# Optimization experiments

Hardware: AMD Instinct MI355X
Metric: run time of the kernel (lower is better)

Reference implementation:

```python
import jax, jax.numpy as jnp
import numpy as np

N_TGT = 100000
DEG = 16
N_EDGE = N_TGT * DEG
N_NBR = 200000
F_IN = 128
F_OUT = 128


def setup_inputs() -> dict:
    key = jax.random.key(0)
    k1, k2, k3, k4, k5, k6 = jax.random.split(key, 6)
    csr_row_ptr = (jnp.arange(N_TGT + 1, dtype=jnp.int64 if jax.config.x64_enabled else jnp.int32) * DEG).astype(jnp.int32)
    csr_col_ind = jax.random.randint(k1, (N_EDGE,), 0, N_NBR, dtype=jnp.int32)
    sample_count = jax.random.randint(k2, (N_NBR,), 0, DEG, dtype=jnp.int32)
    x_neighboor = jax.random.normal(k3, (N_NBR, F_IN), dtype=jnp.float32)
    x_target = jax.random.normal(k4, (N_TGT, F_IN), dtype=jnp.float32)
    # Linear(in=2*F_IN, out=F_OUT): xavier_uniform weight (gain for relu = sqrt(2)),
    # default torch Linear bias init U(-1/sqrt(fan_in), 1/sqrt(fan_in)).
    fan_in = 2 * F_IN
    gain = float(np.sqrt(2.0))
    bound_w = gain * float(np.sqrt(6.0 / (fan_in + F_OUT)))
    lin_weight = jax.random.uniform(k5, (F_OUT, fan_in), dtype=jnp.float32, minval=-bound_w, maxval=bound_w)
    bound_b = 1.0 / float(np.sqrt(fan_in))
    lin_bias = jax.random.uniform(k6, (F_OUT,), dtype=jnp.float32, minval=-bound_b, maxval=bound_b)
    bias = jnp.zeros((F_OUT,), dtype=jnp.float32)  # extra self.bias Parameter (zeros)
    return {
        "csr_row_ptr": csr_row_ptr,
        "csr_col_ind": csr_col_ind,
        "sample_count": sample_count,
        "x_neighboor": x_neighboor,
        "x_target": x_target,
        "lin_weight": lin_weight,
        "lin_bias": lin_bias,
        "bias": bias,
    }


def _mean_aggregate(csr_row_ptr, csr_col_ind, x_neighboor):
    n_tgt = csr_row_ptr.shape[0] - 1
    n_edge = csr_col_ind.shape[0]
    # row id for each edge: which CSR segment it falls into
    edge_ids = jnp.arange(n_edge, dtype=csr_row_ptr.dtype)
    row_ids = jnp.searchsorted(csr_row_ptr, edge_ids, side="right") - 1
    gathered = x_neighboor[csr_col_ind]                      # [E, F]
    summed = jax.ops.segment_sum(gathered, row_ids, num_segments=n_tgt)  # [N, F]
    counts = (csr_row_ptr[1:] - csr_row_ptr[:-1]).astype(x_neighboor.dtype)
    counts = jnp.maximum(counts, 1.0)
    return summed / counts[:, None]


def reference(csr_row_ptr, csr_col_ind, sample_count, x_neighboor, x_target, lin_weight, lin_bias, bias):
    agg = _mean_aggregate(csr_row_ptr, csr_col_ind, x_neighboor)        # [N, F_IN]
    cat = jnp.concatenate([x_target, agg], axis=1)                       # [N, 2*F_IN]
    y = cat @ lin_weight.T + lin_bias
    y = y + bias  # module adds its own self.bias on top of Linear's bias
    return y
```

## Files before the change

kernel.cpp:

```cpp
#include <hip/hip_runtime.h>

#define TM 64
#define F_INC 128
#define K_DIM 256
#define F_OUTC 128
#define CAT_LD 264

using fv2    = __attribute__((ext_vector_type(2))) float;
using fv4    = __attribute__((ext_vector_type(4))) float;
using f32x4  = __attribute__((ext_vector_type(4))) float;
using bf16x8 = __attribute__((ext_vector_type(8))) short;
using u16x8  = __attribute__((ext_vector_type(8))) unsigned short;

static __device__ __forceinline__ unsigned short f2bf(float f) {
    union { float f; unsigned u; } v; v.f = f;
    unsigned u = v.u;
    u += 0x7FFFu + ((u >> 16) & 1u);
    return (unsigned short)(u >> 16);
}

__global__ __launch_bounds__(256) void f32_to_bf16_kernel(
    const float* __restrict__ src, unsigned short* __restrict__ dst, int n8)
{
    const int i = blockIdx.x * 256 + threadIdx.x;
    if (i < n8) {
        const fv4 a = *(const fv4*)(src + (size_t)i * 8);
        const fv4 b = *(const fv4*)(src + (size_t)i * 8 + 4);
        u16x8 o;
        o[0] = f2bf(a[0]); o[1] = f2bf(a[1]); o[2] = f2bf(a[2]); o[3] = f2bf(a[3]);
        o[4] = f2bf(b[0]); o[5] = f2bf(b[1]); o[6] = f2bf(b[2]); o[7] = f2bf(b[3]);
        *(u16x8*)(dst + (size_t)i * 8) = o;
    }
}

__global__ __launch_bounds__(256) void f32_to_fp8_kernel(
    const float* __restrict__ src, unsigned int* __restrict__ dst, int n8)
{
    const int i = blockIdx.x * 256 + threadIdx.x;
    if (i < n8) {
        const fv4 a = *(const fv4*)(src + (size_t)i * 8);
        const fv4 b = *(const fv4*)(src + (size_t)i * 8 + 4);
        unsigned int w0 = (unsigned)__builtin_amdgcn_cvt_pk_fp8_f32(a[0], a[1], 0, false);
        w0 = (unsigned)__builtin_amdgcn_cvt_pk_fp8_f32(a[2], a[3], (int)w0, true);
        unsigned int w1 = (unsigned)__builtin_amdgcn_cvt_pk_fp8_f32(b[0], b[1], 0, false);
        w1 = (unsigned)__builtin_amdgcn_cvt_pk_fp8_f32(b[2], b[3], (int)w1, true);
        uint2 o; o.x = w0; o.y = w1;
        *(uint2*)(dst + (size_t)i * 2) = o;
    }
}

template <int USE_WS>
__global__ __launch_bounds__(256) void sage_fused_kernel(
    const int* __restrict__ row_ptr,
    const int* __restrict__ col_ind,
    const float* __restrict__ x_nbr,
    const unsigned int* __restrict__ nbr_f8,
    const float* __restrict__ x_tgt,
    const float* __restrict__ w,
    const unsigned short* __restrict__ w_bf,
    const float* __restrict__ lin_b,
    const float* __restrict__ bias,
    float* __restrict__ out,
    int n_tgt)
{
    __shared__ int s_ptr[TM + 1];
    __shared__ int s_idx[TM * 16];
    __shared__ unsigned short s_cat[TM][CAT_LD];

    const int tid = threadIdx.x;
    const int g0  = blockIdx.x * TM;

    if (tid < TM + 1) {
        int gp = g0 + tid;
        if (gp > n_tgt) gp = n_tgt;
        s_ptr[tid] = row_ptr[gp];
    }
    __syncthreads();

    for (int e = tid; e < TM * 16; e += 256) {
        const int m = e >> 4, j = e & 15;
        const int start = s_ptr[m];
        const int deg = s_ptr[m + 1] - start;
        s_idx[e] = (j < deg) ? col_ind[start + j] : 0;
    }
    __syncthreads();

    if (USE_WS) {
        const int team = tid >> 3;
        const int lt   = tid & 7;
        for (int mi = 0; mi < 2; ++mi) {
            const int m  = team + mi * 32;
            const int gm = g0 + m;
            {
                u16x8 t0 = {0,0,0,0,0,0,0,0}, t1 = {0,0,0,0,0,0,0,0};
                if (gm < n_tgt) {
                    const float* tp = x_tgt + (size_t)gm * F_INC + lt * 16;
                    const fv4 a = *(const fv4*)(tp);
                    const fv4 b = *(const fv4*)(tp + 4);
                    const fv4 c = *(const fv4*)(tp + 8);
                    const fv4 d = *(const fv4*)(tp + 12);
                    t0[0]=f2bf(a[0]); t0[1]=f2bf(a[1]); t0[2]=f2bf(a[2]); t0[3]=f2bf(a[3]);
                    t0[4]=f2bf(b[0]); t0[5]=f2bf(b[1]); t0[6]=f2bf(b[2]); t0[7]=f2bf(b[3]);
                    t1[0]=f2bf(c[0]); t1[1]=f2bf(c[1]); t1[2]=f2bf(c[2]); t1[3]=f2bf(c[3]);
                    t1[4]=f2bf(d[0]); t1[5]=f2bf(d[1]); t1[6]=f2bf(d[2]); t1[7]=f2bf(d[3]);
                }
                *(u16x8*)&s_cat[m][lt * 16]     = t0;
                *(u16x8*)&s_cat[m][lt * 16 + 8] = t1;
            }
            const int deg = s_ptr[m + 1] - s_ptr[m];
            float acc[16];
#pragma unroll
            for (int i = 0; i < 16; ++i) acc[i] = 0.f;
            const int* idx = &s_idx[m * 16];
            if (deg == 16) {
#pragma unroll
                for (int j = 0; j < 16; ++j) {
                    const uint4 v = *(const uint4*)(nbr_f8 + (size_t)idx[j] * 32 + lt * 4);
                    fv2 p;
                    p = __builtin_amdgcn_cvt_pk_f32_fp8(v.x, false); acc[0]+=p[0];  acc[1]+=p[1];
                    p = __builtin_amdgcn_cvt_pk_f32_fp8(v.x, true ); acc[2]+=p[0];  acc[3]+=p[1];
                    p = __builtin_amdgcn_cvt_pk_f32_fp8(v.y, false); acc[4]+=p[0];  acc[5]+=p[1];
                    p = __builtin_amdgcn_cvt_pk_f32_fp8(v.y, true ); acc[6]+=p[0];  acc[7]+=p[1];
                    p = __builtin_amdgcn_cvt_pk_f32_fp8(v.z, false); acc[8]+=p[0];  acc[9]+=p[1];
                    p = __builtin_amdgcn_cvt_pk_f32_fp8(v.z, true ); acc[10]+=p[0]; acc[11]+=p[1];
                    p = __builtin_amdgcn_cvt_pk_f32_fp8(v.w, false); acc[12]+=p[0]; acc[13]+=p[1];
                    p = __builtin_amdgcn_cvt_pk_f32_fp8(v.w, true ); acc[14]+=p[0]; acc[15]+=p[1];
                }
            } else {
                for (int j = 0; j < deg; ++j) {
                    const uint4 v = *(const uint4*)(nbr_f8 + (size_t)idx[j] * 32 + lt * 4);
                    fv2 p;
                    p = __builtin_amdgcn_cvt_pk_f32_fp8(v.x, false); acc[0]+=p[0];  acc[1]+=p[1];
                    p = __builtin_amdgcn_cvt_pk_f32_fp8(v.x, true ); acc[2]+=p[0];  acc[3]+=p[1];
                    p = __builtin_amdgcn_cvt_pk_f32_fp8(v.y, false); acc[4]+=p[0];  acc[5]+=p[1];
                    p = __builtin_amdgcn_cvt_pk_f32_fp8(v.y, true ); acc[6]+=p[0];  acc[7]+=p[1];
                    p = __builtin_amdgcn_cvt_pk_f32_fp8(v.z, false); acc[8]+=p[0];  acc[9]+=p[1];
                    p = __builtin_amdgcn_cvt_pk_f32_fp8(v.z, true ); acc[10]+=p[0]; acc[11]+=p[1];
                    p = __builtin_amdgcn_cvt_pk_f32_fp8(v.w, false); acc[12]+=p[0]; acc[13]+=p[1];
                    p = __builtin_amdgcn_cvt_pk_f32_fp8(v.w, true ); acc[14]+=p[0]; acc[15]+=p[1];
                }
            }
            const float sc = 1.0f / (float)(deg > 0 ? deg : 1);
            u16x8 p0, p1;
#pragma unroll
            for (int i = 0; i < 8; ++i) { p0[i] = f2bf(acc[i] * sc); p1[i] = f2bf(acc[8 + i] * sc); }
            *(u16x8*)&s_cat[m][128 + lt * 16]     = p0;
            *(u16x8*)&s_cat[m][128 + lt * 16 + 8] = p1;
        }
    } else {
        const int lane32 = tid & 31;
        const int grp = tid >> 5;
        for (int m = grp; m < TM; m += 8) {
            const int gm = g0 + m;
            fv4 t = {0.f, 0.f, 0.f, 0.f};
            if (gm < n_tgt)
                t = *(const fv4*)(x_tgt + (size_t)gm * F_INC + lane32 * 4);
            {
                ushort4 p;
                p.x = f2bf(t[0]); p.y = f2bf(t[1]); p.z = f2bf(t[2]); p.w = f2bf(t[3]);
                *(ushort4*)&s_cat[m][lane32 * 4] = p;
            }
            const int deg = s_ptr[m + 1] - s_ptr[m];
            fv4 acc = {0.f, 0.f, 0.f, 0.f};
            const int* idx = &s_idx[m * 16];
            if (deg == 16) {
#pragma unroll
                for (int j = 0; j < 16; ++j)
                    acc += *(const fv4*)(x_nbr + (size_t)idx[j] * F_INC + lane32 * 4);
            } else {
                for (int j = 0; j < deg; ++j)
                    acc += *(const fv4*)(x_nbr + (size_t)idx[j] * F_INC + lane32 * 4);
            }
            const float sc = 1.0f / (float)(deg > 0 ? deg : 1);
            acc *= sc;
            {
                ushort4 p;
                p.x = f2bf(acc[0]); p.y = f2bf(acc[1]); p.z = f2bf(acc[2]); p.w = f2bf(acc[3]);
                *(ushort4*)&s_cat[m][128 + lane32 * 4] = p;
            }
        }
    }
    __syncthreads();

    const int lane = tid & 63;
    const int wave = tid >> 6;
    const int col  = lane & 15;
    const int kq   = lane >> 4;
    const int r0   = kq * 4;

    bf16x8 bfr[2][8];
#pragma unroll
    for (int h = 0; h < 2; ++h) {
        const int o = h * 64 + wave * 16 + col;
#pragma unroll
        for (int kt = 0; kt < 8; ++kt) {
            if (USE_WS) {
                bfr[h][kt] = *(const bf16x8*)(w_bf + (size_t)o * K_DIM + kt * 32 + kq * 8);
            } else {
                const float* p = w + (size_t)o * K_DIM + kt * 32 + kq * 8;
                fv4 lo = *(const fv4*)p;
                fv4 hi = *(const fv4*)(p + 4);
                bf16x8 b;
                b[0] = (short)f2bf(lo[0]); b[1] = (short)f2bf(lo[1]);
                b[2] = (short)f2bf(lo[2]); b[3] = (short)f2bf(lo[3]);
                b[4] = (short)f2bf(hi[0]); b[5] = (short)f2bf(hi[1]);
                b[6] = (short)f2bf(hi[2]); b[7] = (short)f2bf(hi[3]);
                bfr[h][kt] = b;
            }
        }
    }

    const int o0 = wave * 16 + col;
    const int o1 = 64 + o0;
    const float bs0 = lin_b[o0] + bias[o0];
    const float bs1 = lin_b[o1] + bias[o1];

#pragma unroll 1
    for (int mt = 0; mt < 4; ++mt) {
        const int mrow = mt * 16 + col;
        bf16x8 afr[8];
#pragma unroll
        for (int kt = 0; kt < 8; ++kt)
            afr[kt] = *(const bf16x8*)&s_cat[mrow][kt * 32 + kq * 8];

        f32x4 acc0 = {0.f, 0.f, 0.f, 0.f};
        f32x4 acc1 = {0.f, 0.f, 0.f, 0.f};
#pragma unroll
        for (int kt = 0; kt < 8; ++kt) {
            acc0 = __builtin_amdgcn_mfma_f32_16x16x32_bf16(afr[kt], bfr[0][kt], acc0, 0, 0, 0);
            acc1 = __builtin_amdgcn_mfma_f32_16x16x32_bf16(afr[kt], bfr[1][kt], acc1, 0, 0, 0);
        }

#pragma unroll
        for (int i = 0; i < 4; ++i) {
            const int gm = g0 + mt * 16 + r0 + i;
            if (gm < n_tgt) {
                out[(size_t)gm * F_OUTC + o0] = acc0[i] + bs0;
                out[(size_t)gm * F_OUTC + o1] = acc1[i] + bs1;
            }
        }
    }
}

extern "C" void kernel_launch(void* const* d_in, const int* in_sizes, int n_in,
                              void* d_out, int out_size, void* d_ws, size_t ws_size,
                              hipStream_t stream) {
    const int*   row_ptr = (const int*)d_in[0];
    const int*   col_ind = (const int*)d_in[1];
    const float* x_nbr   = (const float*)d_in[3];
    const float* x_tgt   = (const float*)d_in[4];
    const float* w       = (const float*)d_in[5];
    const float* lb      = (const float*)d_in[6];
    const float* bs      = (const float*)d_in[7];
    float* out = (float*)d_out;

    const int n_tgt  = in_sizes[0] - 1;
    const int n_nbrf = in_sizes[3];
    const int n_wf   = in_sizes[5];
    const int grid   = (n_tgt + TM - 1) / TM;

    const size_t nbr_bytes = (size_t)n_nbrf;
    const size_t need = nbr_bytes + (size_t)n_wf * 2;

    if (ws_size >= need) {
        unsigned int*   nbr_f8 = (unsigned int*)d_ws;
        unsigned short* w_bf   = (unsigned short*)((char*)d_ws + nbr_bytes);
        const int n8n = n_nbrf / 8;
        const int n8w = n_wf / 8;
        hipLaunchKernelGGL(f32_to_fp8_kernel, dim3((n8n + 255) / 256), dim3(256), 0, stream,
                           x_nbr, nbr_f8, n8n);
        hipLaunchKernelGGL(f32_to_bf16_kernel, dim3((n8w + 255) / 256), dim3(256), 0, stream,
                           w, w_bf, n8w);
        hipLaunchKernelGGL(sage_fused_kernel<1>, dim3(grid), dim3(256), 0, stream,
                           row_ptr, col_ind, x_nbr, nbr_f8, x_tgt, w, w_bf, lb, bs, out, n_tgt);
    } else {
        hipLaunchKernelGGL(sage_fused_kernel<0>, dim3(grid), dim3(256), 0, stream,
                           row_ptr, col_ind, x_nbr, (const unsigned int*)nullptr,
                           x_tgt, w, (const unsigned short*)nullptr, lb, bs, out, n_tgt);
    }
}
```

Baseline: 84.33 us.

## Halve target tile, merge conversion kernels, cut register use in MFMA stage

Merges the fp8 neighbour conversion and the bf16 weight conversion into a single launch, which removes one kernel launch. Halves the per-block target tile to 32 rows, so each thread gathers one row instead of two and the grid doubles. The MFMA stage now keeps only one half of the weight fragments live at a time and loads A fragments inside the loop, which lowers register pressure to raise occupancy. The cost is that each block loads the weights and biases for half as many rows, so weight reloads per output row double.

```diff
diff --git a/kernel.cpp b/kernel.cpp
--- a/kernel.cpp
+++ b/kernel.cpp
@@ -1,6 +1,6 @@
 #include <hip/hip_runtime.h>
 
-#define TM 64
+#define TM 32
 #define F_INC 128
 #define K_DIM 256
 #define F_OUTC 128
@@ -19,33 +19,30 @@
     return (unsigned short)(u >> 16);
 }
 
-__global__ __launch_bounds__(256) void f32_to_bf16_kernel(
-    const float* __restrict__ src, unsigned short* __restrict__ dst, int n8)
+__global__ __launch_bounds__(256) void convert_kernel(
+    const float* __restrict__ xn, unsigned int* __restrict__ nf8, int n8n,
+    const float* __restrict__ w, unsigned short* __restrict__ wbf, int n8w)
 {
     const int i = blockIdx.x * 256 + threadIdx.x;
-    if (i < n8) {
-        const fv4 a = *(const fv4*)(src + (size_t)i * 8);
-        const fv4 b = *(const fv4*)(src + (size_t)i * 8 + 4);
-        u16x8 o;
-        o[0] = f2bf(a[0]); o[1] = f2bf(a[1]); o[2] = f2bf(a[2]); o[3] = f2bf(a[3]);
-        o[4] = f2bf(b[0]); o[5] = f2bf(b[1]); o[6] = f2bf(b[2]); o[7] = f2bf(b[3]);
-        *(u16x8*)(dst + (size_t)i * 8) = o;
-    }
-}
-
-__global__ __launch_bounds__(256) void f32_to_fp8_kernel(
-    const float* __restrict__ src, unsigned int* __restrict__ dst, int n8)
-{
-    const int i = blockIdx.x * 256 + threadIdx.x;
-    if (i < n8) {
-        const fv4 a = *(const fv4*)(src + (size_t)i * 8);
-        const fv4 b = *(const fv4*)(src + (size_t)i * 8 + 4);
+    if (i < n8n) {
+        const fv4 a = *(const fv4*)(xn + (size_t)i * 8);
+        const fv4 b = *(const fv4*)(xn + (size_t)i * 8 + 4);
         unsigned int w0 = (unsigned)__builtin_amdgcn_cvt_pk_fp8_f32(a[0], a[1], 0, false);
         w0 = (unsigned)__builtin_amdgcn_cvt_pk_fp8_f32(a[2], a[3], (int)w0, true);
         unsigned int w1 = (unsigned)__builtin_amdgcn_cvt_pk_fp8_f32(b[0], b[1], 0, false);
         w1 = (unsigned)__builtin_amdgcn_cvt_pk_fp8_f32(b[2], b[3], (int)w1, true);
         uint2 o; o.x = w0; o.y = w1;
-        *(uint2*)(dst + (size_t)i * 2) = o;
+        *(uint2*)(nf8 + (size_t)i * 2) = o;
+    } else {
+        const int j = i - n8n;
+        if (j < n8w) {
+            const fv4 a = *(const fv4*)(w + (size_t)j * 8);
+            const fv4 b = *(const fv4*)(w + (size_t)j * 8 + 4);
+            u16x8 o;
+            o[0] = f2bf(a[0]); o[1] = f2bf(a[1]); o[2] = f2bf(a[2]); o[3] = f2bf(a[3]);
+            o[4] = f2bf(b[0]); o[5] = f2bf(b[1]); o[6] = f2bf(b[2]); o[7] = f2bf(b[3]);
+            *(u16x8*)(wbf + (size_t)j * 8) = o;
+        }
     }
 }
 
@@ -77,7 +74,9 @@
     }
     __syncthreads();
 
-    for (int e = tid; e < TM * 16; e += 256) {
+#pragma unroll
+    for (int e0 = 0; e0 < TM * 16; e0 += 256) {
+        const int e = e0 + tid;
         const int m = e >> 4, j = e & 15;
         const int start = s_ptr[m];
         const int deg = s_ptr[m + 1] - start;
@@ -86,67 +85,64 @@
     __syncthreads();
 
     if (USE_WS) {
-        const int team = tid >> 3;
-        const int lt   = tid & 7;
-        for (int mi = 0; mi < 2; ++mi) {
-            const int m  = team + mi * 32;
-            const int gm = g0 + m;
-            {
-                u16x8 t0 = {0,0,0,0,0,0,0,0}, t1 = {0,0,0,0,0,0,0,0};
-                if (gm < n_tgt) {
-                    const float* tp = x_tgt + (size_t)gm * F_INC + lt * 16;
-                    const fv4 a = *(const fv4*)(tp);
-                    const fv4 b = *(const fv4*)(tp + 4);
-                    const fv4 c = *(const fv4*)(tp + 8);
-                    const fv4 d = *(const fv4*)(tp + 12);
-                    t0[0]=f2bf(a[0]); t0[1]=f2bf(a[1]); t0[2]=f2bf(a[2]); t0[3]=f2bf(a[3]);
-                    t0[4]=f2bf(b[0]); t0[5]=f2bf(b[1]); t0[6]=f2bf(b[2]); t0[7]=f2bf(b[3]);
-                    t1[0]=f2bf(c[0]); t1[1]=f2bf(c[1]); t1[2]=f2bf(c[2]); t1[3]=f2bf(c[3]);
-                    t1[4]=f2bf(d[0]); t1[5]=f2bf(d[1]); t1[6]=f2bf(d[2]); t1[7]=f2bf(d[3]);
-                }
-                *(u16x8*)&s_cat[m][lt * 16]     = t0;
-                *(u16x8*)&s_cat[m][lt * 16 + 8] = t1;
-            }
-            const int deg = s_ptr[m + 1] - s_ptr[m];
-            float acc[16];
-#pragma unroll
-            for (int i = 0; i < 16; ++i) acc[i] = 0.f;
-            const int* idx = &s_idx[m * 16];
-            if (deg == 16) {
-#pragma unroll
-                for (int j = 0; j < 16; ++j) {
-                    const uint4 v = *(const uint4*)(nbr_f8 + (size_t)idx[j] * 32 + lt * 4);
-                    fv2 p;
-                    p = __builtin_amdgcn_cvt_pk_f32_fp8(v.x, false); acc[0]+=p[0];  acc[1]+=p[1];
-                    p = __builtin_amdgcn_cvt_pk_f32_fp8(v.x, true ); acc[2]+=p[0];  acc[3]+=p[1];
-                    p = __builtin_amdgcn_cvt_pk_f32_fp8(v.y, false); acc[4]+=p[0];  acc[5]+=p[1];
-                    p = __builtin_amdgcn_cvt_pk_f32_fp8(v.y, true ); acc[6]+=p[0];  acc[7]+=p[1];
-                    p = __builtin_amdgcn_cvt_pk_f32_fp8(v.z, false); acc[8]+=p[0];  acc[9]+=p[1];
-                    p = __builtin_amdgcn_cvt_pk_f32_fp8(v.z, true ); acc[10]+=p[0]; acc[11]+=p[1];
-                    p = __builtin_amdgcn_cvt_pk_f32_fp8(v.w, false); acc[12]+=p[0]; acc[13]+=p[1];
-                    p = __builtin_amdgcn_cvt_pk_f32_fp8(v.w, true ); acc[14]+=p[0]; acc[15]+=p[1];
-                }
-            } else {
-                for (int j = 0; j < deg; ++j) {
-                    const uint4 v = *(const uint4*)(nbr_f8 + (size_t)idx[j] * 32 + lt * 4);
-                    fv2 p;
-                    p = __builtin_amdgcn_cvt_pk_f32_fp8(v.x, false); acc[0]+=p[0];  acc[1]+=p[1];
-                    p = __builtin_amdgcn_cvt_pk_f32_fp8(v.x, true ); acc[2]+=p[0];  acc[3]+=p[1];
-                    p = __builtin_amdgcn_cvt_pk_f32_fp8(v.y, false); acc[4]+=p[0];  acc[5]+=p[1];
-                    p = __builtin_amdgcn_cvt_pk_f32_fp8(v.y, true ); acc[6]+=p[0];  acc[7]+=p[1];
-                    p = __builtin_amdgcn_cvt_pk_f32_fp8(v.z, false); acc[8]+=p[0];  acc[9]+=p[1];
-                    p = __builtin_amdgcn_cvt_pk_f32_fp8(v.z, true ); acc[10]+=p[0]; acc[11]+=p[1];
-                    p = __builtin_amdgcn_cvt_pk_f32_fp8(v.w, false); acc[12]+=p[0]; acc[13]+=p[1];
-                    p = __builtin_amdgcn_cvt_pk_f32_fp8(v.w, true ); acc[14]+=p[0]; acc[15]+=p[1];
-                }
-            }
-            const float sc = 1.0f / (float)(deg > 0 ? deg : 1);
-            u16x8 p0, p1;
-#pragma unroll
-            for (int i = 0; i < 8; ++i) { p0[i] = f2bf(acc[i] * sc); p1[i] = f2bf(acc[8 + i] * sc); }
-            *(u16x8*)&s_cat[m][128 + lt * 16]     = p0;
-            *(u16x8*)&s_cat[m][128 + lt * 16 + 8] = p1;
-        }
+        const int m  = tid >> 3;
+        const int lt = tid & 7;
+        const int gm = g0 + m;
+        {
+            u16x8 t0 = {0,0,0,0,0,0,0,0}, t1 = {0,0,0,0,0,0,0,0};
+            if (gm < n_tgt) {
+                const float* tp = x_tgt + (size_t)gm * F_INC + lt * 16;
+                const fv4 a = *(const fv4*)(tp);
+                const fv4 b = *(const fv4*)(tp + 4);
+                const fv4 c = *(const fv4*)(tp + 8);
+                const fv4 d = *(const fv4*)(tp + 12);
+                t0[0]=f2bf(a[0]); t0[1]=f2bf(a[1]); t0[2]=f2bf(a[2]); t0[3]=f2bf(a[3]);
+                t0[4]=f2bf(b[0]); t0[5]=f2bf(b[1]); t0[6]=f2bf(b[2]); t0[7]=f2bf(b[3]);
+                t1[0]=f2bf(c[0]); t1[1]=f2bf(c[1]); t1[2]=f2bf(c[2]); t1[3]=f2bf(c[3]);
+                t1[4]=f2bf(d[0]); t1[5]=f2bf(d[1]); t1[6]=f2bf(d[2]); t1[7]=f2bf(d[3]);
+            }
+            *(u16x8*)&s_cat[m][lt * 16]     = t0;
+            *(u16x8*)&s_cat[m][lt * 16 + 8] = t1;
+        }
+        const int deg = s_ptr[m + 1] - s_ptr[m];
+        float acc[16];
+#pragma unroll
+        for (int i = 0; i < 16; ++i) acc[i] = 0.f;
+        const int* idx = &s_idx[m * 16];
+        if (deg == 16) {
+#pragma unroll
+            for (int j = 0; j < 16; ++j) {
+                const uint4 v = *(const uint4*)(nbr_f8 + (size_t)idx[j] * 32 + lt * 4);
+                fv2 p;
+                p = __builtin_amdgcn_cvt_pk_f32_fp8(v.x, false); acc[0]+=p[0];  acc[1]+=p[1];
+                p = __builtin_amdgcn_cvt_pk_f32_fp8(v.x, true ); acc[2]+=p[0];  acc[3]+=p[1];
+                p = __builtin_amdgcn_cvt_pk_f32_fp8(v.y, false); acc[4]+=p[0];  acc[5]+=p[1];
+                p = __builtin_amdgcn_cvt_pk_f32_fp8(v.y, true ); acc[6]+=p[0];  acc[7]+=p[1];
+                p = __builtin_amdgcn_cvt_pk_f32_fp8(v.z, false); acc[8]+=p[0];  acc[9]+=p[1];
+                p = __builtin_amdgcn_cvt_pk_f32_fp8(v.z, true ); acc[10]+=p[0]; acc[11]+=p[1];
+                p = __builtin_amdgcn_cvt_pk_f32_fp8(v.w, false); acc[12]+=p[0]; acc[13]+=p[1];
+                p = __builtin_amdgcn_cvt_pk_f32_fp8(v.w, true ); acc[14]+=p[0]; acc[15]+=p[1];
+            }
+        } else {
+            for (int j = 0; j < deg; ++j) {
+                const uint4 v = *(const uint4*)(nbr_f8 + (size_t)idx[j] * 32 + lt * 4);
+                fv2 p;
+                p = __builtin_amdgcn_cvt_pk_f32_fp8(v.x, false); acc[0]+=p[0];  acc[1]+=p[1];
+                p = __builtin_amdgcn_cvt_pk_f32_fp8(v.x, true ); acc[2]+=p[0];  acc[3]+=p[1];
+                p = __builtin_amdgcn_cvt_pk_f32_fp8(v.y, false); acc[4]+=p[0];  acc[5]+=p[1];
+                p = __builtin_amdgcn_cvt_pk_f32_fp8(v.y, true ); acc[6]+=p[0];  acc[7]+=p[1];
+                p = __builtin_amdgcn_cvt_pk_f32_fp8(v.z, false); acc[8]+=p[0];  acc[9]+=p[1];
+                p = __builtin_amdgcn_cvt_pk_f32_fp8(v.z, true ); acc[10]+=p[0]; acc[11]+=p[1];
+                p = __builtin_amdgcn_cvt_pk_f32_fp8(v.w, false); acc[12]+=p[0]; acc[13]+=p[1];
+                p = __builtin_amdgcn_cvt_pk_f32_fp8(v.w, true ); acc[14]+=p[0]; acc[15]+=p[1];
+            }
+        }
+        const float sc = 1.0f / (float)(deg > 0 ? deg : 1);
+        u16x8 p0, p1;
+#pragma unroll
+        for (int i = 0; i < 8; ++i) { p0[i] = f2bf(acc[i] * sc); p1[i] = f2bf(acc[8 + i] * sc); }
+        *(u16x8*)&s_cat[m][128 + lt * 16]     = p0;
+        *(u16x8*)&s_cat[m][128 + lt * 16 + 8] = p1;
     } else {
         const int lane32 = tid & 31;
         const int grp = tid >> 5;
@@ -187,15 +183,16 @@
     const int col  = lane & 15;
     const int kq   = lane >> 4;
     const int r0   = kq * 4;
-
-    bf16x8 bfr[2][8];
-#pragma unroll
+    const int o_base = wave * 16 + col;
+
+#pragma unroll 1
     for (int h = 0; h < 2; ++h) {
-        const int o = h * 64 + wave * 16 + col;
+        const int o = h * 64 + o_base;
+        bf16x8 bfr[8];
 #pragma unroll
         for (int kt = 0; kt < 8; ++kt) {
             if (USE_WS) {
-                bfr[h][kt] = *(const bf16x8*)(w_bf + (size_t)o * K_DIM + kt * 32 + kq * 8);
+                bfr[kt] = *(const bf16x8*)(w_bf + (size_t)o * K_DIM + kt * 32 + kq * 8);
             } else {
                 const float* p = w + (size_t)o * K_DIM + kt * 32 + kq * 8;
                 fv4 lo = *(const fv4*)p;
@@ -205,38 +202,25 @@
                 b[2] = (short)f2bf(lo[2]); b[3] = (short)f2bf(lo[3]);
                 b[4] = (short)f2bf(hi[0]); b[5] = (short)f2bf(hi[1]);
                 b[6] = (short)f2bf(hi[2]); b[7] = (short)f2bf(hi[3]);
-                bfr[h][kt] = b;
-            }
-        }
-    }
-
-    const int o0 = wave * 16 + col;
-    const int o1 = 64 + o0;
-    const float bs0 = lin_b[o0] + bias[o0];
-    const float bs1 = lin_b[o1] + bias[o1];
-
-#pragma unroll 1
-    for (int mt = 0; mt < 4; ++mt) {
-        const int mrow = mt * 16 + col;
-        bf16x8 afr[8];
-#pragma unroll
-        for (int kt = 0; kt < 8; ++kt)
-            afr[kt] = *(const bf16x8*)&s_cat[mrow][kt * 32 + kq * 8];
-
-        f32x4 acc0 = {0.f, 0.f, 0.f, 0.f};
-        f32x4 acc1 = {0.f, 0.f, 0.f, 0.f};
-#pragma unroll
-        for (int kt = 0; kt < 8; ++kt) {
-            acc0 = __builtin_amdgcn_mfma_f32_16x16x32_bf16(afr[kt], bfr[0][kt], acc0, 0, 0, 0);
-            acc1 = __builtin_amdgcn_mfma_f32_16x16x32_bf16(afr[kt], bfr[1][kt], acc1, 0, 0, 0);
-        }
-
-#pragma unroll
-        for (int i = 0; i < 4; ++i) {
-            const int gm = g0 + mt * 16 + r0 + i;
-            if (gm < n_tgt) {
-                out[(size_t)gm * F_OUTC + o0] = acc0[i] + bs0;
-                out[(size_t)gm * F_OUTC + o1] = acc1[i] + bs1;
+                bfr[kt] = b;
+            }
+        }
+        const float bs = lin_b[o] + bias[o];
+
+#pragma unroll
+        for (int mt = 0; mt < 2; ++mt) {
+            const int mrow = mt * 16 + col;
+            f32x4 acc = {0.f, 0.f, 0.f, 0.f};
+#pragma unroll
+            for (int kt = 0; kt < 8; ++kt) {
+                const bf16x8 afr = *(const bf16x8*)&s_cat[mrow][kt * 32 + kq * 8];
+                acc = __builtin_amdgcn_mfma_f32_16x16x32_bf16(afr, bfr[kt], acc, 0, 0, 0);
+            }
+#pragma unroll
+            for (int i = 0; i < 4; ++i) {
+                const int gm = g0 + mt * 16 + r0 + i;
+                if (gm < n_tgt)
+                    out[(size_t)gm * F_OUTC + o] = acc[i] + bs;
             }
         }
     }
@@ -267,10 +251,9 @@
         unsigned short* w_bf   = (unsigned short*)((char*)d_ws + nbr_bytes);
         const int n8n = n_nbrf / 8;
         const int n8w = n_wf / 8;
-        hipLaunchKernelGGL(f32_to_fp8_kernel, dim3((n8n + 255) / 256), dim3(256), 0, stream,
-                           x_nbr, nbr_f8, n8n);
-        hipLaunchKernelGGL(f32_to_bf16_kernel, dim3((n8w + 255) / 256), dim3(256), 0, stream,
-                           w, w_bf, n8w);
+        const int cblocks = (n8n + n8w + 255) / 256;
+        hipLaunchKernelGGL(convert_kernel, dim3(cblocks), dim3(256), 0, stream,
+                           x_nbr, nbr_f8, n8n, w, w_bf, n8w);
         hipLaunchKernelGGL(sage_fused_kernel<1>, dim3(grid), dim3(256), 0, stream,
                            row_ptr, col_ind, x_nbr, nbr_f8, x_tgt, w, w_bf, lb, bs, out, n_tgt);
     } else {
```

After: 95.40 us. 13.1% more time.

## Restructure MFMA epilogue to hold one weight half at a time

Applied to the files above, without the earlier changes.

The GEMM stage now loops over the two output-column halves, keeping only 8 bf16 weight fragments in registers instead of 16 and re-reading the A fragments from LDS for each half. This is meant to lower VGPR pressure and so raise occupancy, which helps the latency-bound gather. The cost is twice the LDS reads of the concatenated tile. The change also drops the specialised fully-unrolled degree-16 gather path, which may reduce memory-level parallelism in the fallback path, and adds unroll pragmas to the index-staging and target-conversion loops.

```diff
diff --git a/kernel.cpp b/kernel.cpp
--- a/kernel.cpp
+++ b/kernel.cpp
@@ -77,7 +77,9 @@
     }
     __syncthreads();
 
-    for (int e = tid; e < TM * 16; e += 256) {
+#pragma unroll
+    for (int e0 = 0; e0 < TM * 16; e0 += 256) {
+        const int e = e0 + tid;
         const int m = e >> 4, j = e & 15;
         const int start = s_ptr[m];
         const int deg = s_ptr[m + 1] - start;
@@ -88,6 +90,7 @@
     if (USE_WS) {
         const int team = tid >> 3;
         const int lt   = tid & 7;
+#pragma unroll
         for (int mi = 0; mi < 2; ++mi) {
             const int m  = team + mi * 32;
             const int gm = g0 + m;
@@ -163,14 +166,8 @@
             const int deg = s_ptr[m + 1] - s_ptr[m];
             fv4 acc = {0.f, 0.f, 0.f, 0.f};
             const int* idx = &s_idx[m * 16];
-            if (deg == 16) {
-#pragma unroll
-                for (int j = 0; j < 16; ++j)
-                    acc += *(const fv4*)(x_nbr + (size_t)idx[j] * F_INC + lane32 * 4);
-            } else {
-                for (int j = 0; j < deg; ++j)
-                    acc += *(const fv4*)(x_nbr + (size_t)idx[j] * F_INC + lane32 * 4);
-            }
+            for (int j = 0; j < deg; ++j)
+                acc += *(const fv4*)(x_nbr + (size_t)idx[j] * F_INC + lane32 * 4);
             const float sc = 1.0f / (float)(deg > 0 ? deg : 1);
             acc *= sc;
             {
@@ -187,15 +184,16 @@
     const int col  = lane & 15;
     const int kq   = lane >> 4;
     const int r0   = kq * 4;
-
-    bf16x8 bfr[2][8];
-#pragma unroll
+    const int o_base = wave * 16 + col;
+
+#pragma unroll 1
     for (int h = 0; h < 2; ++h) {
-        const int o = h * 64 + wave * 16 + col;
+        const int o = h * 64 + o_base;
+        bf16x8 bfr[8];
 #pragma unroll
         for (int kt = 0; kt < 8; ++kt) {
             if (USE_WS) {
-                bfr[h][kt] = *(const bf16x8*)(w_bf + (size_t)o * K_DIM + kt * 32 + kq * 8);
+                bfr[kt] = *(const bf16x8*)(w_bf + (size_t)o * K_DIM + kt * 32 + kq * 8);
             } else {
                 const float* p = w + (size_t)o * K_DIM + kt * 32 + kq * 8;
                 fv4 lo = *(const fv4*)p;
@@ -205,38 +203,25 @@
                 b[2] = (short)f2bf(lo[2]); b[3] = (short)f2bf(lo[3]);
                 b[4] = (short)f2bf(hi[0]); b[5] = (short)f2bf(hi[1]);
                 b[6] = (short)f2bf(hi[2]); b[7] = (short)f2bf(hi[3]);
-                bfr[h][kt] = b;
-            }
-        }
-    }
-
-    const int o0 = wave * 16 + col;
-    const int o1 = 64 + o0;
-    const float bs0 = lin_b[o0] + bias[o0];
-    const float bs1 = lin_b[o1] + bias[o1];
-
-#pragma unroll 1
-    for (int mt = 0; mt < 4; ++mt) {
-        const int mrow = mt * 16 + col;
-        bf16x8 afr[8];
-#pragma unroll
-        for (int kt = 0; kt < 8; ++kt)
-            afr[kt] = *(const bf16x8*)&s_cat[mrow][kt * 32 + kq * 8];
-
-        f32x4 acc0 = {0.f, 0.f, 0.f, 0.f};
-        f32x4 acc1 = {0.f, 0.f, 0.f, 0.f};
-#pragma unroll
-        for (int kt = 0; kt < 8; ++kt) {
-            acc0 = __builtin_amdgcn_mfma_f32_16x16x32_bf16(afr[kt], bfr[0][kt], acc0, 0, 0, 0);
-            acc1 = __builtin_amdgcn_mfma_f32_16x16x32_bf16(afr[kt], bfr[1][kt], acc1, 0, 0, 0);
-        }
-
-#pragma unroll
-        for (int i = 0; i < 4; ++i) {
-            const int gm = g0 + mt * 16 + r0 + i;
-            if (gm < n_tgt) {
-                out[(size_t)gm * F_OUTC + o0] = acc0[i] + bs0;
-                out[(size_t)gm * F_OUTC + o1] = acc1[i] + bs1;
+                bfr[kt] = b;
+            }
+        }
+        const float bs = lin_b[o] + bias[o];
+
+#pragma unroll
+        for (int mt = 0; mt < 4; ++mt) {
+            const int mrow = mt * 16 + col;
+            f32x4 acc = {0.f, 0.f, 0.f, 0.f};
+#pragma unroll
+            for (int kt = 0; kt < 8; ++kt) {
+                const bf16x8 afr = *(const bf16x8*)&s_cat[mrow][kt * 32 + kq * 8];
+                acc = __builtin_amdgcn_mfma_f32_16x16x32_bf16(afr, bfr[kt], acc, 0, 0, 0);
+            }
+#pragma unroll
+            for (int i = 0; i < 4; ++i) {
+                const int gm = g0 + mt * 16 + r0 + i;
+                if (gm < n_tgt)
+                    out[(size_t)gm * F_OUTC + o] = acc[i] + bs;
             }
         }
     }
```

Measured after the change: 87.64 us. 3.9% more time.
